# Kernel tuning notes

Hardware: AMD Instinct MI355X
Metric: run time of the kernel (lower is better)

Reference implementation:

```python
import jax, jax.numpy as jnp
import numpy as np

RADIUS = 0.1
K = 32  # num_neighbors


def _ball_query(points, centers, radius, k):
    # points: [B,3,N], centers: [B,3,M] -> indices [B,M,K] (int32)
    # PVCNN semantics: first k point indices within radius of each center,
    # unfilled slots padded with the first in-ball index (0 if none in ball).
    N = points.shape[-1]
    p2 = jnp.sum(points * points, axis=1)            # [B,N]
    c2 = jnp.sum(centers * centers, axis=1)          # [B,M]
    cp = jnp.einsum('bdm,bdn->bmn', centers, points)  # [B,M,N]
    dist2 = c2[:, :, None] + p2[:, None, :] - 2.0 * cp
    valid = dist2 < radius * radius                  # [B,M,N]
    # score = point index if in ball else sentinel N; sorting ascending puts
    # the first k in-ball indices (in original point order) up front.
    scores = jnp.where(valid, jnp.arange(N, dtype=jnp.int32), jnp.int32(N))
    idx = jnp.sort(scores, axis=-1)[..., :k]         # [B,M,K]
    first = idx[..., :1]
    first = jnp.where(first == N, 0, first)          # no neighbor -> index 0
    return jnp.where(idx == N, first, idx)


def _group(feat, idx):
    # feat: [B,C,N], idx: [B,M,K] -> [B,C,M,K]
    return jnp.take_along_axis(feat[:, :, None, :], idx[:, None, :, :], axis=3)


def setup_inputs() -> dict:
    key = jax.random.key(0)
    k1, k2, k3 = jax.random.split(key, 3)
    B, N, M, C = 2, 16384, 4096, 32
    points_coords = jax.random.uniform(k1, (B, 3, N), dtype=jnp.float32)
    centers_coords = jax.random.uniform(k2, (B, 3, M), dtype=jnp.float32)
    points_features = jax.random.normal(k3, (B, C, N), dtype=jnp.float32)
    return {
        'points_coords': points_coords,
        'centers_coords': centers_coords,
        'points_features': points_features,
    }


def reference(points_coords, centers_coords, points_features):
    idx = _ball_query(points_coords, centers_coords, RADIUS, K)     # [B,M,K]
    nbr_coords = _group(points_coords, idx)                          # [B,3,M,K]
    nbr_coords = nbr_coords - centers_coords[:, :, :, None]         # relative
    nbr_feats = _group(points_features, idx)                         # [B,C,M,K]
    out = jnp.concatenate([nbr_coords, nbr_feats], axis=1)          # [B,3+C,M,K]
    return jnp.transpose(out, (0, 1, 3, 2))                          # [B,3+C,K,M]
```

## Files before the change

### kernel.cpp

```cpp
#include <hip/hip_runtime.h>

#define B_SZ  2
#define N_PTS 16384
#define M_CTR 4096
#define C_FT  32
#define K_NB  32
#define NCH   35
#define CH_STRIDE (K_NB * M_CTR)
#define CELLS 10
#define NCELL (CELLS * CELLS * CELLS)

__device__ __forceinline__ float fmul(float a, float b) {
    float r; asm("v_mul_f32 %0, %1, %2" : "=v"(r) : "v"(a), "v"(b)); return r;
}
__device__ __forceinline__ float fadd(float a, float b) {
    float r; asm("v_add_f32 %0, %1, %2" : "=v"(r) : "v"(a), "v"(b)); return r;
}
__device__ __forceinline__ float fsub(float a, float b) {
    float r; asm("v_sub_f32 %0, %1, %2" : "=v"(r) : "v"(a), "v"(b)); return r;
}
__device__ __forceinline__ float ffma(float a, float b, float c) {
    float r; asm("v_fma_f32 %0, %1, %2, %3" : "=v"(r) : "v"(a), "v"(b), "v"(c));
    return r;
}

__device__ __forceinline__ bool bq_valid(float x, float y, float z,
                                         float cx, float cy, float cz,
                                         float c2, float r2) {
    const float p2 = fadd(fadd(fmul(x, x), fmul(y, y)), fmul(z, z));
    const float cp = ffma(cz, z, ffma(cy, y, fmul(cx, x)));
    return fsub(fadd(c2, p2), fmul(2.0f, cp)) < r2;
}

__device__ __forceinline__ int cell_of(float x, float y, float z) {
    int ci = (int)(x * 10.0f); ci = ci < 0 ? 0 : (ci > 9 ? 9 : ci);
    int cj = (int)(y * 10.0f); cj = cj < 0 ? 0 : (cj > 9 ? 9 : cj);
    int ck = (int)(z * 10.0f); ck = ck < 0 ? 0 : (ck > 9 ? 9 : ck);
    return (ck * CELLS + cj) * CELLS + ci;
}

__global__ __launch_bounds__(256) void zero_kernel(int* __restrict__ hist) {
    const int t = blockIdx.x * 256 + threadIdx.x;
    if (t < B_SZ * NCELL) hist[t] = 0;
}

__global__ __launch_bounds__(256) void hist_kernel(
    const float* __restrict__ points, int* __restrict__ hist) {
    const int t = blockIdx.x * 256 + threadIdx.x;
    const int b = t >> 14, n = t & (N_PTS - 1);
    const float x = points[(b * 3 + 0) * N_PTS + n];
    const float y = points[(b * 3 + 1) * N_PTS + n];
    const float z = points[(b * 3 + 2) * N_PTS + n];
    atomicAdd(&hist[b * NCELL + cell_of(x, y, z)], 1);
}

__global__ __launch_bounds__(1024) void scan_kernel(
    const int* __restrict__ hist, int* __restrict__ starts,
    int* __restrict__ cursor) {
    __shared__ int s[1024];
    const int t = threadIdx.x;
    for (int b = 0; b < B_SZ; ++b) {
        s[t] = (t < NCELL) ? hist[b * NCELL + t] : 0;
        __syncthreads();
        for (int off = 1; off < 1024; off <<= 1) {
            const int v = (t >= off) ? s[t - off] : 0;
            __syncthreads();
            s[t] += v;
            __syncthreads();
        }
        if (t < NCELL) {
            const int st = (t == 0) ? 0 : s[t - 1];
            starts[b * (NCELL + 1) + t] = st;
            cursor[b * NCELL + t] = st;
        }
        if (t == 0) starts[b * (NCELL + 1) + NCELL] = s[NCELL - 1];
        __syncthreads();
    }
}

__global__ __launch_bounds__(256) void scatter_kernel(
    const float* __restrict__ points, int* __restrict__ cursor,
    float4* __restrict__ binned) {
    const int t = blockIdx.x * 256 + threadIdx.x;
    const int b = t >> 14, n = t & (N_PTS - 1);
    const float x = points[(b * 3 + 0) * N_PTS + n];
    const float y = points[(b * 3 + 1) * N_PTS + n];
    const float z = points[(b * 3 + 2) * N_PTS + n];
    const int pos = atomicAdd(&cursor[b * NCELL + cell_of(x, y, z)], 1);
    binned[b * N_PTS + pos] = make_float4(x, y, z, __int_as_float(n));
}

__global__ __launch_bounds__(256) void ball_query_kernel(
    const float4* __restrict__ binned,
    const float* __restrict__ centers,
    const int* __restrict__ starts,
    int* __restrict__ idx_out)
{
    const int lane = threadIdx.x & 63;
    const int wid  = threadIdx.x >> 6;
    const int cid  = blockIdx.x * 4 + wid;
    const int b = cid >> 12;
    const int m = cid & (M_CTR - 1);

    const float r2 = (float)(0.1 * 0.1);

    const float cx = centers[(b * 3 + 0) * M_CTR + m];
    const float cy = centers[(b * 3 + 1) * M_CTR + m];
    const float cz = centers[(b * 3 + 2) * M_CTR + m];
    const float c2 = fadd(fadd(fmul(cx, cx), fmul(cy, cy)), fmul(cz, cz));

    __shared__ unsigned bitmap[4][N_PTS / 32];
    unsigned* bm = bitmap[wid];
#pragma unroll
    for (int j = 0; j < 8; ++j) bm[lane * 8 + j] = 0u;

    int ci = (int)(cx * 10.0f); ci = ci < 0 ? 0 : (ci > 9 ? 9 : ci);
    int cj = (int)(cy * 10.0f); cj = cj < 0 ? 0 : (cj > 9 ? 9 : cj);
    int ck = (int)(cz * 10.0f); ck = ck < 0 ? 0 : (ck > 9 ? 9 : ck);
    const int i0 = ci > 0 ? ci - 1 : 0;
    const int i1 = ci < 9 ? ci + 1 : 9;
    const int* st = starts + b * (NCELL + 1);
    const float4* __restrict__ bp = binned + b * N_PTS;

    for (int d = 0; d < 9; ++d) {
        const int jj = cj + (d % 3) - 1;
        const int kk = ck + (d / 3) - 1;
        if (jj < 0 || jj > 9 || kk < 0 || kk > 9) continue;
        const int base = (kk * CELLS + jj) * CELLS;
        const int lo = st[base + i0];
        const int hi = st[base + i1 + 1];
        for (int s0 = lo; s0 < hi; s0 += 64) {
            const int t = s0 + lane;
            if (t < hi) {
                const float4 p = bp[t];
                if (bq_valid(p.x, p.y, p.z, cx, cy, cz, c2, r2)) {
                    const int n = __float_as_int(p.w);
                    atomicOr((int*)&bm[n >> 5], 1 << (n & 31));
                }
            }
        }
    }

    unsigned w[8];
    int cnt = 0;
#pragma unroll
    for (int j = 0; j < 8; ++j) { w[j] = bm[lane * 8 + j]; cnt += __popc(w[j]); }

    int incl = cnt;
    for (int off = 1; off < 64; off <<= 1) {
        const int v = __shfl_up(incl, off);
        if (lane >= off) incl += v;
    }
    const int total = __shfl(incl, 63);
    int slot = incl - cnt;

    int firstbit = 0x7fffffff;
#pragma unroll
    for (int j = 0; j < 8; ++j) {
        if (w[j] && firstbit == 0x7fffffff)
            firstbit = lane * 256 + j * 32 + (__ffs(w[j]) - 1);
    }
    for (int off = 32; off > 0; off >>= 1)
        firstbit = min(firstbit, __shfl_xor(firstbit, off));
    const int first_idx = (total == 0) ? 0 : firstbit;

    int* __restrict__ dst = idx_out + (b * K_NB) * M_CTR + m;
#pragma unroll
    for (int j = 0; j < 8; ++j) {
        unsigned x = w[j];
        while (x && slot < K_NB) {
            const int bit = __ffs(x) - 1;
            dst[slot * M_CTR] = lane * 256 + j * 32 + bit;
            x &= x - 1;
            ++slot;
        }
    }
    if (lane >= total && lane < K_NB) dst[lane * M_CTR] = first_idx;
}

__global__ __launch_bounds__(256) void transpose_kernel(
    const float* __restrict__ points,
    const float* __restrict__ feats,
    float* __restrict__ pf)
{
    __shared__ float tile[64][37];
    const int t  = threadIdx.x;
    const int b  = blockIdx.x >> 8;
    const int n0 = (blockIdx.x & 255) * 64;

    for (int i = t; i < NCH * 64; i += 256) {
        const int r = i >> 6;
        const int c = i & 63;
        float v;
        if (r < 3) v = points[(b * 3 + r) * N_PTS + n0 + c];
        else       v = feats[(b * C_FT + (r - 3)) * N_PTS + n0 + c];
        tile[c][r] = v;
    }
    if (t < 64) tile[t][35] = 0.0f;
    __syncthreads();

    float* __restrict__ dst = pf + ((size_t)b * N_PTS + n0) * 36;
    for (int o = t; o < 64 * 36; o += 256) {
        const int c = o / 36;
        const int r = o - c * 36;
        dst[o] = tile[c][r];
    }
}

__global__ __launch_bounds__(256) void gather_kernel(
    const float* __restrict__ pf,
    const float* __restrict__ centers,
    const int* __restrict__ idx,
    float* __restrict__ out)
{
    const int t = blockIdx.x * 256 + threadIdx.x;
    const int m = t & (M_CTR - 1);
    const int k = (t >> 12) & (K_NB - 1);
    const int b = t >> 17;

    const int n = idx[(b * K_NB + k) * M_CTR + m];
    const float4* __restrict__ src = (const float4*)(pf + ((size_t)b * N_PTS + n) * 36);

    float4 f[9];
#pragma unroll
    for (int i = 0; i < 9; ++i) f[i] = src[i];

    const float cx = centers[(b * 3 + 0) * M_CTR + m];
    const float cy = centers[(b * 3 + 1) * M_CTR + m];
    const float cz = centers[(b * 3 + 2) * M_CTR + m];

    float vv[36];
#pragma unroll
    for (int i = 0; i < 9; ++i) {
        vv[4 * i + 0] = f[i].x; vv[4 * i + 1] = f[i].y;
        vv[4 * i + 2] = f[i].z; vv[4 * i + 3] = f[i].w;
    }
    vv[0] -= cx; vv[1] -= cy; vv[2] -= cz;

    float* __restrict__ o = out + ((size_t)b * NCH * K_NB + k) * M_CTR + m;
#pragma unroll
    for (int ch = 0; ch < NCH; ++ch)
        o[(size_t)ch * CH_STRIDE] = vv[ch];
}

extern "C" void kernel_launch(void* const* d_in, const int* in_sizes, int n_in,
                              void* d_out, int out_size, void* d_ws, size_t ws_size,
                              hipStream_t stream) {
    const float* points  = (const float*)d_in[0];
    const float* centers = (const float*)d_in[1];
    const float* feats   = (const float*)d_in[2];
    float* out = (float*)d_out;

    char* ws = (char*)d_ws;
    int*    idx    = (int*)ws;
    float*  pf     = (float*)(ws + (1u << 20));
    int*    hist   = (int*)(ws + 5700 * 1024);
    int*    cursor = (int*)(ws + 5716 * 1024);
    int*    starts = (int*)(ws + 5732 * 1024);
    float4* binned = (float4*)(ws + 5764 * 1024);

    zero_kernel<<<(B_SZ * NCELL + 255) / 256, 256, 0, stream>>>(hist);
    hist_kernel<<<(B_SZ * N_PTS) / 256, 256, 0, stream>>>(points, hist);
    scan_kernel<<<1, 1024, 0, stream>>>(hist, starts, cursor);
    scatter_kernel<<<(B_SZ * N_PTS) / 256, 256, 0, stream>>>(points, cursor, binned);
    transpose_kernel<<<B_SZ * (N_PTS / 64), 256, 0, stream>>>(points, feats, pf);

    ball_query_kernel<<<(B_SZ * M_CTR) / 4, 256, 0, stream>>>(
        binned, centers, starts, idx);

    const int total = B_SZ * K_NB * M_CTR;
    gather_kernel<<<total / 256, 256, 0, stream>>>(pf, centers, idx, out);
}
```

Baseline: 114.5 us.

## Fuse binning prep into one kernel and vectorize gather to four centers per thread

Replaces the zero, histogram, scan, scatter and transpose kernels with one prep kernel. One block per batch builds the cell histogram in shared memory, runs a wave-shuffle scan and scatters the binned points, while the remaining blocks do the feature transpose. The gather kernel now handles four consecutive centers per thread, using int4 index loads and float4 output stores. This cuts launch count and global atomics and widens stores, but the binning work now runs on only two blocks with serial loops, which may leave it on the critical path.

```diff
diff --git a/kernel.cpp b/kernel.cpp
--- a/kernel.cpp
+++ b/kernel.cpp
@@ -39,55 +39,88 @@
     return (ck * CELLS + cj) * CELLS + ci;
 }
 
-__global__ __launch_bounds__(256) void zero_kernel(int* __restrict__ hist) {
-    const int t = blockIdx.x * 256 + threadIdx.x;
-    if (t < B_SZ * NCELL) hist[t] = 0;
-}
-
-__global__ __launch_bounds__(256) void hist_kernel(
-    const float* __restrict__ points, int* __restrict__ hist) {
-    const int t = blockIdx.x * 256 + threadIdx.x;
-    const int b = t >> 14, n = t & (N_PTS - 1);
-    const float x = points[(b * 3 + 0) * N_PTS + n];
-    const float y = points[(b * 3 + 1) * N_PTS + n];
-    const float z = points[(b * 3 + 2) * N_PTS + n];
-    atomicAdd(&hist[b * NCELL + cell_of(x, y, z)], 1);
-}
-
-__global__ __launch_bounds__(1024) void scan_kernel(
-    const int* __restrict__ hist, int* __restrict__ starts,
-    int* __restrict__ cursor) {
-    __shared__ int s[1024];
-    const int t = threadIdx.x;
-    for (int b = 0; b < B_SZ; ++b) {
-        s[t] = (t < NCELL) ? hist[b * NCELL + t] : 0;
-        __syncthreads();
-        for (int off = 1; off < 1024; off <<= 1) {
-            const int v = (t >= off) ? s[t - off] : 0;
-            __syncthreads();
-            s[t] += v;
-            __syncthreads();
-        }
-        if (t < NCELL) {
-            const int st = (t == 0) ? 0 : s[t - 1];
-            starts[b * (NCELL + 1) + t] = st;
-            cursor[b * NCELL + t] = st;
-        }
-        if (t == 0) starts[b * (NCELL + 1) + NCELL] = s[NCELL - 1];
-        __syncthreads();
-    }
-}
-
-__global__ __launch_bounds__(256) void scatter_kernel(
-    const float* __restrict__ points, int* __restrict__ cursor,
-    float4* __restrict__ binned) {
-    const int t = blockIdx.x * 256 + threadIdx.x;
-    const int b = t >> 14, n = t & (N_PTS - 1);
-    const float x = points[(b * 3 + 0) * N_PTS + n];
-    const float y = points[(b * 3 + 1) * N_PTS + n];
-    const float z = points[(b * 3 + 2) * N_PTS + n];
-    const int pos = atomicAdd(&cursor[b * NCELL + cell_of(x, y, z)], 1);
-    binned[b * N_PTS + pos] = make_float4(x, y, z, __int_as_float(n));
+__global__ __launch_bounds__(256) void prep_kernel(
+    const float* __restrict__ points,
+    const float* __restrict__ feats,
+    float4* __restrict__ binned,
+    int* __restrict__ starts,
+    float* __restrict__ pf)
+{
+    if (blockIdx.x < B_SZ) {
+        const int b = blockIdx.x;
+        const int t = threadIdx.x;
+        const int lane = t & 63, wid = t >> 6;
+        __shared__ int h[NCELL];
+        __shared__ int cur[NCELL];
+        __shared__ int wsum[4];
+        for (int c = t; c < NCELL; c += 256) h[c] = 0;
+        __syncthreads();
+
+        const float* __restrict__ px = points + (b * 3 + 0) * N_PTS;
+        const float* __restrict__ py = points + (b * 3 + 1) * N_PTS;
+        const float* __restrict__ pz = points + (b * 3 + 2) * N_PTS;
+
+#pragma unroll 4
+        for (int i = 0; i < 64; ++i) {
+            const int n = t + i * 256;
+            atomicAdd(&h[cell_of(px[n], py[n], pz[n])], 1);
+        }
+        __syncthreads();
+
+        const int c0 = t * 4;
+        int h0 = 0, h1 = 0, h2 = 0, h3 = 0;
+        if (c0 < NCELL) { h0 = h[c0]; h1 = h[c0+1]; h2 = h[c0+2]; h3 = h[c0+3]; }
+        const int s = h0 + h1 + h2 + h3;
+        int incl = s;
+        for (int off = 1; off < 64; off <<= 1) {
+            const int u = __shfl_up(incl, off);
+            if (lane >= off) incl += u;
+        }
+        if (lane == 63) wsum[wid] = incl;
+        __syncthreads();
+        const int woff = (wid > 0 ? wsum[0] : 0) + (wid > 1 ? wsum[1] : 0)
+                       + (wid > 2 ? wsum[2] : 0);
+        if (c0 < NCELL) {
+            int e = incl - s + woff;
+            int* st = starts + b * (NCELL + 1);
+            st[c0] = e;     cur[c0] = e;     e += h0;
+            st[c0+1] = e;   cur[c0+1] = e;   e += h1;
+            st[c0+2] = e;   cur[c0+2] = e;   e += h2;
+            st[c0+3] = e;   cur[c0+3] = e;   e += h3;
+            if (c0 + 4 == NCELL) st[NCELL] = e;
+        }
+        __syncthreads();
+
+#pragma unroll 4
+        for (int i = 0; i < 64; ++i) {
+            const int n = t + i * 256;
+            const float x = px[n], y = py[n], z = pz[n];
+            const int pos = atomicAdd(&cur[cell_of(x, y, z)], 1);
+            binned[b * N_PTS + pos] = make_float4(x, y, z, __int_as_float(n));
+        }
+    } else {
+        __shared__ float tile[64][37];
+        const int bid = blockIdx.x - B_SZ;
+        const int t  = threadIdx.x;
+        const int b  = bid >> 8;
+        const int n0 = (bid & 255) * 64;
+        for (int i = t; i < NCH * 64; i += 256) {
+            const int r = i >> 6;
+            const int c = i & 63;
+            float v;
+            if (r < 3) v = points[(b * 3 + r) * N_PTS + n0 + c];
+            else       v = feats[(b * C_FT + (r - 3)) * N_PTS + n0 + c];
+            tile[c][r] = v;
+        }
+        if (t < 64) tile[t][35] = 0.0f;
+        __syncthreads();
+        float* __restrict__ dst = pf + ((size_t)b * N_PTS + n0) * 36;
+        for (int o = t; o < 64 * 36; o += 256) {
+            const int c = o / 36;
+            const int r = o - c * 36;
+            dst[o] = tile[c][r];
+        }
+    }
 }
 
 __global__ __launch_bounds__(256) void ball_query_kernel(
@@ -178,35 +211,6 @@
     if (lane >= total && lane < K_NB) dst[lane * M_CTR] = first_idx;
 }
 
-__global__ __launch_bounds__(256) void transpose_kernel(
-    const float* __restrict__ points,
-    const float* __restrict__ feats,
-    float* __restrict__ pf)
-{
-    __shared__ float tile[64][37];
-    const int t  = threadIdx.x;
-    const int b  = blockIdx.x >> 8;
-    const int n0 = (blockIdx.x & 255) * 64;
-
-    for (int i = t; i < NCH * 64; i += 256) {
-        const int r = i >> 6;
-        const int c = i & 63;
-        float v;
-        if (r < 3) v = points[(b * 3 + r) * N_PTS + n0 + c];
-        else       v = feats[(b * C_FT + (r - 3)) * N_PTS + n0 + c];
-        tile[c][r] = v;
-    }
-    if (t < 64) tile[t][35] = 0.0f;
-    __syncthreads();
-
-    float* __restrict__ dst = pf + ((size_t)b * N_PTS + n0) * 36;
-    for (int o = t; o < 64 * 36; o += 256) {
-        const int c = o / 36;
-        const int r = o - c * 36;
-        dst[o] = tile[c][r];
-    }
-}
-
 __global__ __launch_bounds__(256) void gather_kernel(
     const float* __restrict__ pf,
     const float* __restrict__ centers,
@@ -214,33 +218,37 @@
     float* __restrict__ out)
 {
     const int t = blockIdx.x * 256 + threadIdx.x;
-    const int m = t & (M_CTR - 1);
-    const int k = (t >> 12) & (K_NB - 1);
-    const int b = t >> 17;
-
-    const int n = idx[(b * K_NB + k) * M_CTR + m];
-    const float4* __restrict__ src = (const float4*)(pf + ((size_t)b * N_PTS + n) * 36);
-
-    float4 f[9];
-#pragma unroll
-    for (int i = 0; i < 9; ++i) f[i] = src[i];
-
-    const float cx = centers[(b * 3 + 0) * M_CTR + m];
-    const float cy = centers[(b * 3 + 1) * M_CTR + m];
-    const float cz = centers[(b * 3 + 2) * M_CTR + m];
-
-    float vv[36];
-#pragma unroll
-    for (int i = 0; i < 9; ++i) {
-        vv[4 * i + 0] = f[i].x; vv[4 * i + 1] = f[i].y;
-        vv[4 * i + 2] = f[i].z; vv[4 * i + 3] = f[i].w;
-    }
-    vv[0] -= cx; vv[1] -= cy; vv[2] -= cz;
+    const int m = (t & (M_CTR / 4 - 1)) * 4;
+    const int k = (t >> 10) & (K_NB - 1);
+    const int b = t >> 15;
+
+    const int4 nn = *(const int4*)&idx[(b * K_NB + k) * M_CTR + m];
+    const float4* __restrict__ r0 = (const float4*)(pf + ((size_t)b * N_PTS + nn.x) * 36);
+    const float4* __restrict__ r1 = (const float4*)(pf + ((size_t)b * N_PTS + nn.y) * 36);
+    const float4* __restrict__ r2 = (const float4*)(pf + ((size_t)b * N_PTS + nn.z) * 36);
+    const float4* __restrict__ r3 = (const float4*)(pf + ((size_t)b * N_PTS + nn.w) * 36);
+
+    const float4 cx = *(const float4*)&centers[(b * 3 + 0) * M_CTR + m];
+    const float4 cy = *(const float4*)&centers[(b * 3 + 1) * M_CTR + m];
+    const float4 cz = *(const float4*)&centers[(b * 3 + 2) * M_CTR + m];
 
     float* __restrict__ o = out + ((size_t)b * NCH * K_NB + k) * M_CTR + m;
-#pragma unroll
-    for (int ch = 0; ch < NCH; ++ch)
-        o[(size_t)ch * CH_STRIDE] = vv[ch];
+
+#pragma unroll
+    for (int g = 0; g < 9; ++g) {
+        float4 a = r0[g], e = r1[g], f = r2[g], h = r3[g];
+        if (g == 0) {
+            a.x -= cx.x; a.y -= cy.x; a.z -= cz.x;
+            e.x -= cx.y; e.y -= cy.y; e.z -= cz.y;
+            f.x -= cx.z; f.y -= cy.z; f.z -= cz.z;
+            h.x -= cx.w; h.y -= cy.w; h.z -= cz.w;
+        }
+        *(float4*)&o[(size_t)(4 * g + 0) * CH_STRIDE] = make_float4(a.x, e.x, f.x, h.x);
+        *(float4*)&o[(size_t)(4 * g + 1) * CH_STRIDE] = make_float4(a.y, e.y, f.y, h.y);
+        *(float4*)&o[(size_t)(4 * g + 2) * CH_STRIDE] = make_float4(a.z, e.z, f.z, h.z);
+        if (g < 8)
+            *(float4*)&o[(size_t)(4 * g + 3) * CH_STRIDE] = make_float4(a.w, e.w, f.w, h.w);
+    }
 }
 
 extern "C" void kernel_launch(void* const* d_in, const int* in_sizes, int n_in,
@@ -254,20 +262,13 @@
     char* ws = (char*)d_ws;
     int*    idx    = (int*)ws;
     float*  pf     = (float*)(ws + (1u << 20));
-    int*    hist   = (int*)(ws + 5700 * 1024);
-    int*    cursor = (int*)(ws + 5716 * 1024);
     int*    starts = (int*)(ws + 5732 * 1024);
     float4* binned = (float4*)(ws + 5764 * 1024);
 
-    zero_kernel<<<(B_SZ * NCELL + 255) / 256, 256, 0, stream>>>(hist);
-    hist_kernel<<<(B_SZ * N_PTS) / 256, 256, 0, stream>>>(points, hist);
-    scan_kernel<<<1, 1024, 0, stream>>>(hist, starts, cursor);
-    scatter_kernel<<<(B_SZ * N_PTS) / 256, 256, 0, stream>>>(points, cursor, binned);
-    transpose_kernel<<<B_SZ * (N_PTS / 64), 256, 0, stream>>>(points, feats, pf);
-
+    prep_kernel<<<B_SZ + B_SZ * (N_PTS / 64), 256, 0, stream>>>(
+        points, feats, binned, starts, pf);
     ball_query_kernel<<<(B_SZ * M_CTR) / 4, 256, 0, stream>>>(
         binned, centers, starts, idx);
-
-    const int total = B_SZ * K_NB * M_CTR;
-    gather_kernel<<<total / 256, 256, 0, stream>>>(pf, centers, idx, out);
-}
+    gather_kernel<<<(B_SZ * K_NB * M_CTR / 4) / 256, 256, 0, stream>>>(
+        pf, centers, idx, out);
+}
```

New measurement: 127.4 us. 1.11x slower.
